# Kernel tuning notes

Measured on AMD Instinct MI355X. Metric: run time of the kernel, lower is better.

Reference implementation:

```python
import jax, jax.numpy as jnp
import numpy as np

B, S, P, V, D = 8, 32, 8, 8000, 128
CONC = 5.0  # concentrator_factor
EPS = 1e-8  # torch cosine_similarity eps


def setup_inputs() -> dict:
    key = jax.random.key(0)
    ks = jax.random.split(key, 8)
    concepts = jax.random.randint(ks[0], (B, S, P), 0, V)
    concepts_length = jax.random.randint(ks[1], (B, S), 0, P + 1)
    seg_len = jax.random.randint(ks[2], (B,), 1, S + 1)
    embed_w = jax.random.normal(ks[3], (V, D), jnp.float32)
    embed_kb_w = jax.random.normal(ks[4], (V, D), jnp.float32)
    edge_matrix = jax.random.uniform(ks[5], (V, V), jnp.float32)
    affectiveness = jax.random.uniform(ks[6], (V,), jnp.float32)
    lam = jnp.full((V,), 0.5, jnp.float32)  # _lambda init to GAW
    return dict(concepts=concepts, concepts_length=concepts_length, seg_len=seg_len,
                embed_w=embed_w, embed_kb_w=embed_kb_w, edge_matrix=edge_matrix,
                affectiveness=affectiveness, lam=lam)


def reference(concepts, concepts_length, seg_len, embed_w, embed_kb_w,
              edge_matrix, affectiveness, lam):
    f32 = embed_w.dtype
    # init_params: normalize edge_matrix rows by their range
    rng = edge_matrix.max(axis=1) - edge_matrix.min(axis=1)  # [V]
    em = edge_matrix / (rng + (rng == 0).astype(f32))[:, None]

    ce = embed_w[concepts]  # [B,S,P,D]
    # ragged mean over P (empty -> zeros, matching empty_tensor)
    pmask = (jnp.arange(P)[None, None, :] < concepts_length[:, :, None]).astype(f32)  # [B,S,P]
    denom = jnp.maximum(concepts_length, 1).astype(f32)[:, :, None]  # [B,S,1]
    mean_j = (ce * pmask[..., None]).sum(axis=2) / denom  # [B,S,D]
    # mean over valid segments j < seg_len
    smask = (jnp.arange(S)[None, :] < seg_len[:, None]).astype(f32)  # [B,S]
    context = (mean_j * smask[..., None]).sum(axis=1) / seg_len.astype(f32)[:, None]  # [B,D]

    # abs cosine similarity vs KB embedding table
    cn = context / jnp.maximum(jnp.linalg.norm(context, axis=1, keepdims=True), EPS)
    kn = embed_kb_w / jnp.maximum(jnp.linalg.norm(embed_kb_w, axis=1, keepdims=True), EPS)
    cos = jnp.abs(cn @ kn.T)  # [B,V]

    eg = em[concepts]  # [B,S,P,V] irregular row gather
    rel = eg * cos[:, None, None, :]
    aff = (eg > 0).astype(f32) * affectiveness
    w = lam * rel + (1.0 - lam) * aff  # [B,S,P,V]
    attn = jax.nn.softmax(w * CONC, axis=3)
    ce2 = attn @ embed_kb_w  # [B,S,P,D]

    # ragged mean over P again, zero out segments j >= seg_len (padded output)
    out = (ce2 * pmask[..., None]).sum(axis=2) / denom  # [B,S,D]
    out = out * smask[..., None]
    return out
```

## Files before the change

### kernel.cpp

```cpp
#include <hip/hip_runtime.h>
#include <cmath>

#define NB 8
#define NS 32
#define NP 8
#define NV 8000
#define ND 128
#define CONC 5.0f
#define EPS 1e-8f

#define NBS (NB * NS)
#define TROWS 8
#define USPLIT 25
#define URANGE 320
#define UCHUNK 64
#define NCHUNK (URANGE / UCHUNK)
#define ST 12
#define MAXIDX (NB * NS * NP)

#define WS_SCALE  0
#define WS_CN     2048
#define WS_COS    3072
#define WS_MEANJ  67072
#define WS_P      99840

__global__ void k_mean(const int* __restrict__ concepts,
                       const int* __restrict__ concepts_length,
                       const float* __restrict__ embed_w,
                       float* __restrict__ mean_j,
                       float* __restrict__ out) {
    const int bs = blockIdx.x;
    const int d = threadIdx.x;
    out[bs * ND + d] = 0.0f;
    const int len = concepts_length[bs];
    float sum = 0.0f;
    for (int p = 0; p < len; ++p) {
        const int c = concepts[bs * NP + p];
        sum += embed_w[(size_t)c * ND + d];
    }
    mean_j[(size_t)bs * ND + d] = sum / (float)(len > 0 ? len : 1);
}

__global__ void k_ctx2(const int* __restrict__ seg_len,
                       const float* __restrict__ mean_j,
                       float* __restrict__ cn) {
    const int b = blockIdx.x;
    const int d = threadIdx.x;
    const int sl = seg_len[b];
    float acc = 0.0f;
    for (int s = 0; s < sl; ++s) acc += mean_j[(size_t)(b * NS + s) * ND + d];
    acc /= (float)sl;
    float ss = acc * acc;
    #pragma unroll
    for (int m = 1; m < 64; m <<= 1) ss += __shfl_xor(ss, m);
    __shared__ float sred[2];
    if ((d & 63) == 0) sred[d >> 6] = ss;
    __syncthreads();
    const float tot = sred[0] + sred[1];
    cn[b * ND + d] = acc / fmaxf(sqrtf(tot), EPS);
}

__global__ __launch_bounds__(256) void k_cos(const float* __restrict__ kb,
                                             const float* __restrict__ cn,
                                             float* __restrict__ cos_bv) {
    __shared__ float s_cn[NB * ND];
    const int t = threadIdx.x;
    for (int i = t; i < NB * ND; i += 256) s_cn[i] = cn[i];
    __syncthreads();

    const int v = blockIdx.x * 8 + (t >> 5);
    const int l = t & 31;
    const float4 kv = *reinterpret_cast<const float4*>(kb + (size_t)v * ND + (l << 2));
    float ss = kv.x * kv.x + kv.y * kv.y + kv.z * kv.z + kv.w * kv.w;
    #pragma unroll
    for (int m = 1; m < 32; m <<= 1) ss += __shfl_xor(ss, m);
    const float inv = 1.0f / fmaxf(sqrtf(ss), EPS);
    #pragma unroll
    for (int b = 0; b < NB; ++b) {
        const float4 cv = *reinterpret_cast<const float4*>(&s_cn[b * ND + (l << 2)]);
        float dot = kv.x * cv.x + kv.y * cv.y + kv.z * cv.z + kv.w * cv.w;
        #pragma unroll
        for (int m = 1; m < 32; m <<= 1) dot += __shfl_xor(dot, m);
        if (l == 0) cos_bv[b * NV + v] = fabsf(dot * inv);
    }
}

__global__ __launch_bounds__(256) void k_A(
        const int* __restrict__ concepts,
        const int* __restrict__ concepts_length,
        const int* __restrict__ seg_len,
        const float* __restrict__ edge,
        const float* __restrict__ aff,
        const float* __restrict__ lam,
        const float* __restrict__ cos_bv,
        float* __restrict__ f_scale,
        float* __restrict__ pbuf) {
    const int idx = blockIdx.x;
    const int b = idx >> 8;
    const int s = (idx >> 3) & 31;
    const int p = idx & 7;
    if (s >= seg_len[b]) return;
    const int len = concepts_length[b * NS + s];
    if (p >= len) return;
    const int c = concepts[idx];

    const int t = threadIdx.x;
    const float* __restrict__ erow = edge + (size_t)c * NV;
    float4 ev[8];
    float lmax = -INFINITY, lmin = INFINITY;
    #pragma unroll
    for (int k = 0; k < 8; ++k) {
        const int f = t + (k << 8);
        if (f < 2000) {
            const float4 e = *reinterpret_cast<const float4*>(erow + (f << 2));
            ev[k] = e;
            lmax = fmaxf(lmax, fmaxf(fmaxf(e.x, e.y), fmaxf(e.z, e.w)));
            lmin = fminf(lmin, fminf(fminf(e.x, e.y), fminf(e.z, e.w)));
        }
    }
    #pragma unroll
    for (int m = 1; m < 64; m <<= 1) {
        lmax = fmaxf(lmax, __shfl_xor(lmax, m));
        lmin = fminf(lmin, __shfl_xor(lmin, m));
    }
    __shared__ float s_mn[4], s_mx[4], s_sum[4];
    if ((t & 63) == 0) { s_mn[t >> 6] = lmin; s_mx[t >> 6] = lmax; }
    __syncthreads();
    const float rmin = fminf(fminf(s_mn[0], s_mn[1]), fminf(s_mn[2], s_mn[3]));
    const float rmax = fmaxf(fmaxf(s_mx[0], s_mx[1]), fmaxf(s_mx[2], s_mx[3]));
    const float rng = rmax - rmin;
    const float inv_rng = 1.0f / (rng + (rng == 0.0f ? 1.0f : 0.0f));

    const float* __restrict__ cosb = cos_bv + b * NV;
    float* __restrict__ prow = pbuf + (size_t)idx * NV;
    float lsum = 0.0f;
    #pragma unroll
    for (int k = 0; k < 8; ++k) {
        const int f = t + (k << 8);
        if (f < 2000) {
            const int u = f << 2;
            const float4 l4 = *reinterpret_cast<const float4*>(lam + u);
            const float4 a4 = *reinterpret_cast<const float4*>(aff + u);
            const float4 c4 = *reinterpret_cast<const float4*>(cosb + u);
            float4 e = ev[k];
            e.x *= inv_rng; e.y *= inv_rng; e.z *= inv_rng; e.w *= inv_rng;
            float4 pe;
            pe.x = __expf((l4.x * e.x * c4.x + (1.0f - l4.x) * ((e.x > 0.0f) ? 1.0f : 0.0f) * a4.x) * CONC);
            pe.y = __expf((l4.y * e.y * c4.y + (1.0f - l4.y) * ((e.y > 0.0f) ? 1.0f : 0.0f) * a4.y) * CONC);
            pe.z = __expf((l4.z * e.z * c4.z + (1.0f - l4.z) * ((e.z > 0.0f) ? 1.0f : 0.0f) * a4.z) * CONC);
            pe.w = __expf((l4.w * e.w * c4.w + (1.0f - l4.w) * ((e.w > 0.0f) ? 1.0f : 0.0f) * a4.w) * CONC);
            *reinterpret_cast<float4*>(prow + (f << 2)) = pe;
            lsum += pe.x + pe.y + pe.z + pe.w;
        }
    }
    #pragma unroll
    for (int m = 1; m < 64; m <<= 1) lsum += __shfl_xor(lsum, m);
    if ((t & 63) == 0) s_sum[t >> 6] = lsum;
    __syncthreads();
    if (t == 0) {
        const float total = s_sum[0] + s_sum[1] + s_sum[2] + s_sum[3];
        f_scale[idx] = 1.0f / (total * (float)len);
    }
}

__global__ __launch_bounds__(256) void k_B(
        const float* __restrict__ kb,
        const int* __restrict__ seg_len,
        const int* __restrict__ concepts_length,
        const float* __restrict__ f_scale,
        const float* __restrict__ pbuf,
        float* __restrict__ out) {
    const int tile = blockIdx.x;
    const int bs0 = tile * TROWS;
    if ((bs0 & 31) >= seg_len[bs0 >> 5]) return;

    const int t = threadIdx.x;
    const int ug = t & 7;
    const int l = t >> 3;

    __shared__ int   s_ln[TROWS];
    __shared__ float s_sc[TROWS * NP];
    __shared__ __align__(16) float s_p[UCHUNK * ST];

    if (t < TROWS) {
        const int bs = bs0 + t;
        s_ln[t] = ((bs & 31) < seg_len[bs >> 5]) ? concepts_length[bs] : 0;
    }
    if (t < TROWS * NP) {
        const int bs = bs0 + (t >> 3);
        const int p = t & 7;
        const bool valid = ((bs & 31) < seg_len[bs >> 5]) && (p < concepts_length[bs]);
        s_sc[t] = valid ? f_scale[bs * NP + p] : 0.0f;
    }
    __syncthreads();

    const int srow = t >> 5;
    const int sq = t & 31;
    const int lenr = s_ln[srow];
    float scr[NP];
    #pragma unroll
    for (int p = 0; p < NP; ++p) scr[p] = s_sc[srow * NP + p];
    const float* __restrict__ pr = pbuf + (size_t)(bs0 + srow) * NP * NV + (sq << 1);
    const int u0 = blockIdx.y * URANGE;

    float4 acc[TROWS];
    #pragma unroll
    for (int j = 0; j < TROWS; ++j) acc[j] = make_float4(0.f, 0.f, 0.f, 0.f);

    float2 pv = make_float2(0.f, 0.f);
    #pragma unroll
    for (int p = 0; p < NP; ++p)
        if (p < lenr) {
            const float2 v = *reinterpret_cast<const float2*>(pr + (size_t)p * NV + u0);
            pv.x = fmaf(scr[p], v.x, pv.x);
            pv.y = fmaf(scr[p], v.y, pv.y);
        }

    for (int ch = 0; ch < NCHUNK; ++ch) {
        const int uu0 = sq << 1;
        s_p[(uu0 + 0) * ST + srow] = pv.x;
        s_p[(uu0 + 1) * ST + srow] = pv.y;
        float2 pn = make_float2(0.f, 0.f);
        if (ch + 1 < NCHUNK) {
            const int off = u0 + (ch + 1) * UCHUNK;
            #pragma unroll
            for (int p = 0; p < NP; ++p)
                if (p < lenr) {
                    const float2 v = *reinterpret_cast<const float2*>(pr + (size_t)p * NV + off);
                    pn.x = fmaf(scr[p], v.x, pn.x);
                    pn.y = fmaf(scr[p], v.y, pn.y);
                }
        }
        __syncthreads();

        const int uc = u0 + ch * UCHUNK;
        #pragma unroll
        for (int r = 0; r < 8; ++r) {
            const int uu = ug + (r << 3);
            const float4 kv = *reinterpret_cast<const float4*>(
                kb + (size_t)(uc + uu) * ND + (l << 2));
            const float4 p0 = *reinterpret_cast<const float4*>(&s_p[uu * ST]);
            const float4 p1 = *reinterpret_cast<const float4*>(&s_p[uu * ST + 4]);
            acc[0].x = fmaf(p0.x, kv.x, acc[0].x); acc[0].y = fmaf(p0.x, kv.y, acc[0].y);
            acc[0].z = fmaf(p0.x, kv.z, acc[0].z); acc[0].w = fmaf(p0.x, kv.w, acc[0].w);
            acc[1].x = fmaf(p0.y, kv.x, acc[1].x); acc[1].y = fmaf(p0.y, kv.y, acc[1].y);
            acc[1].z = fmaf(p0.y, kv.z, acc[1].z); acc[1].w = fmaf(p0.y, kv.w, acc[1].w);
            acc[2].x = fmaf(p0.z, kv.x, acc[2].x); acc[2].y = fmaf(p0.z, kv.y, acc[2].y);
            acc[2].z = fmaf(p0.z, kv.z, acc[2].z); acc[2].w = fmaf(p0.z, kv.w, acc[2].w);
            acc[3].x = fmaf(p0.w, kv.x, acc[3].x); acc[3].y = fmaf(p0.w, kv.y, acc[3].y);
            acc[3].z = fmaf(p0.w, kv.z, acc[3].z); acc[3].w = fmaf(p0.w, kv.w, acc[3].w);
            acc[4].x = fmaf(p1.x, kv.x, acc[4].x); acc[4].y = fmaf(p1.x, kv.y, acc[4].y);
            acc[4].z = fmaf(p1.x, kv.z, acc[4].z); acc[4].w = fmaf(p1.x, kv.w, acc[4].w);
            acc[5].x = fmaf(p1.y, kv.x, acc[5].x); acc[5].y = fmaf(p1.y, kv.y, acc[5].y);
            acc[5].z = fmaf(p1.y, kv.z, acc[5].z); acc[5].w = fmaf(p1.y, kv.w, acc[5].w);
            acc[6].x = fmaf(p1.z, kv.x, acc[6].x); acc[6].y = fmaf(p1.z, kv.y, acc[6].y);
            acc[6].z = fmaf(p1.z, kv.z, acc[6].z); acc[6].w = fmaf(p1.z, kv.w, acc[6].w);
            acc[7].x = fmaf(p1.w, kv.x, acc[7].x); acc[7].y = fmaf(p1.w, kv.y, acc[7].y);
            acc[7].z = fmaf(p1.w, kv.z, acc[7].z); acc[7].w = fmaf(p1.w, kv.w, acc[7].w);
        }
        __syncthreads();
        pv = pn;
    }

    float4 r0 = make_float4(0.f, 0.f, 0.f, 0.f);
    #pragma unroll
    for (int j = 0; j < TROWS; ++j) {
        float4 a = acc[j];
        #pragma unroll
        for (int m = 1; m <= 4; m <<= 1) {
            a.x += __shfl_xor(a.x, m);
            a.y += __shfl_xor(a.y, m);
            a.z += __shfl_xor(a.z, m);
            a.w += __shfl_xor(a.w, m);
        }
        if (j == ug) r0 = a;
    }

    if (s_ln[ug] != 0) {
        float* o = out + (size_t)(bs0 + ug) * ND + (l << 2);
        atomicAdd(o + 0, r0.x);
        atomicAdd(o + 1, r0.y);
        atomicAdd(o + 2, r0.z);
        atomicAdd(o + 3, r0.w);
    }
}

extern "C" void kernel_launch(void* const* d_in, const int* in_sizes, int n_in,
                              void* d_out, int out_size, void* d_ws, size_t ws_size,
                              hipStream_t stream) {
    const int*   concepts        = (const int*)d_in[0];
    const int*   concepts_length = (const int*)d_in[1];
    const int*   seg_len         = (const int*)d_in[2];
    const float* embed_w         = (const float*)d_in[3];
    const float* embed_kb_w      = (const float*)d_in[4];
    const float* edge_matrix     = (const float*)d_in[5];
    const float* affectiveness   = (const float*)d_in[6];
    const float* lam             = (const float*)d_in[7];
    float* out = (float*)d_out;

    float* wsf = (float*)d_ws;
    float* f_scale  = wsf + WS_SCALE;
    float* cn       = wsf + WS_CN;
    float* cos_bv   = wsf + WS_COS;
    float* mean_j   = wsf + WS_MEANJ;
    float* pbuf     = wsf + WS_P;

    k_mean<<<NB * NS, ND, 0, stream>>>(concepts, concepts_length, embed_w,
                                       mean_j, out);
    k_ctx2<<<NB, ND, 0, stream>>>(seg_len, mean_j, cn);
    k_cos<<<NV / 8, 256, 0, stream>>>(embed_kb_w, cn, cos_bv);
    k_A<<<MAXIDX, 256, 0, stream>>>(concepts, concepts_length, seg_len,
                                    edge_matrix, affectiveness, lam, cos_bv,
                                    f_scale, pbuf);
    dim3 gB(NBS / TROWS, USPLIT, 1);
    k_B<<<gB, 256, 0, stream>>>(embed_kb_w, seg_len, concepts_length,
                                f_scale, pbuf, out);
}
```

Before: 367.8 us.

## Recompute softmax numerators in matmul kernel instead of materializing probability buffer

```diff
diff --git a/kernel.cpp b/kernel.cpp
--- a/kernel.cpp
+++ b/kernel.cpp
@@ -19,10 +19,10 @@
 #define MAXIDX (NB * NS * NP)
 
 #define WS_SCALE  0
-#define WS_CN     2048
-#define WS_COS    3072
-#define WS_MEANJ  67072
-#define WS_P      99840
+#define WS_INVR   2048
+#define WS_CN     4096
+#define WS_COS    5120
+#define WS_MEANJ  69120
 
 __global__ void k_mean(const int* __restrict__ concepts,
                        const int* __restrict__ concepts_length,
@@ -85,7 +85,7 @@
     }
 }
 
-__global__ __launch_bounds__(256) void k_A(
+__global__ __launch_bounds__(256) void k_scale(
         const int* __restrict__ concepts,
         const int* __restrict__ concepts_length,
         const int* __restrict__ seg_len,
@@ -94,7 +94,7 @@
         const float* __restrict__ lam,
         const float* __restrict__ cos_bv,
         float* __restrict__ f_scale,
-        float* __restrict__ pbuf) {
+        float* __restrict__ f_invr) {
     const int idx = blockIdx.x;
     const int b = idx >> 8;
     const int s = (idx >> 3) & 31;
@@ -132,7 +132,6 @@
     const float inv_rng = 1.0f / (rng + (rng == 0.0f ? 1.0f : 0.0f));
 
     const float* __restrict__ cosb = cos_bv + b * NV;
-    float* __restrict__ prow = pbuf + (size_t)idx * NV;
     float lsum = 0.0f;
     #pragma unroll
     for (int k = 0; k < 8; ++k) {
@@ -143,14 +142,13 @@
             const float4 a4 = *reinterpret_cast<const float4*>(aff + u);
             const float4 c4 = *reinterpret_cast<const float4*>(cosb + u);
             float4 e = ev[k];
-            e.x *= inv_rng; e.y *= inv_rng; e.z *= inv_rng; e.w *= inv_rng;
-            float4 pe;
-            pe.x = __expf((l4.x * e.x * c4.x + (1.0f - l4.x) * ((e.x > 0.0f) ? 1.0f : 0.0f) * a4.x) * CONC);
-            pe.y = __expf((l4.y * e.y * c4.y + (1.0f - l4.y) * ((e.y > 0.0f) ? 1.0f : 0.0f) * a4.y) * CONC);
-            pe.z = __expf((l4.z * e.z * c4.z + (1.0f - l4.z) * ((e.z > 0.0f) ? 1.0f : 0.0f) * a4.z) * CONC);
-            pe.w = __expf((l4.w * e.w * c4.w + (1.0f - l4.w) * ((e.w > 0.0f) ? 1.0f : 0.0f) * a4.w) * CONC);
-            *reinterpret_cast<float4*>(prow + (f << 2)) = pe;
-            lsum += pe.x + pe.y + pe.z + pe.w;
+            float4 en;
+            en.x = e.x * inv_rng; en.y = e.y * inv_rng;
+            en.z = e.z * inv_rng; en.w = e.w * inv_rng;
+            lsum += __expf((l4.x * en.x * c4.x + (1.0f - l4.x) * ((e.x > 0.0f) ? 1.0f : 0.0f) * a4.x) * CONC);
+            lsum += __expf((l4.y * en.y * c4.y + (1.0f - l4.y) * ((e.y > 0.0f) ? 1.0f : 0.0f) * a4.y) * CONC);
+            lsum += __expf((l4.z * en.z * c4.z + (1.0f - l4.z) * ((e.z > 0.0f) ? 1.0f : 0.0f) * a4.z) * CONC);
+            lsum += __expf((l4.w * en.w * c4.w + (1.0f - l4.w) * ((e.w > 0.0f) ? 1.0f : 0.0f) * a4.w) * CONC);
         }
     }
     #pragma unroll
@@ -160,47 +158,57 @@
     if (t == 0) {
         const float total = s_sum[0] + s_sum[1] + s_sum[2] + s_sum[3];
         f_scale[idx] = 1.0f / (total * (float)len);
-    }
-}
-
-__global__ __launch_bounds__(256) void k_B(
+        f_invr[idx]  = inv_rng;
+    }
+}
+
+__global__ __launch_bounds__(256) void k_fused(
         const float* __restrict__ kb,
+        const int* __restrict__ concepts,
         const int* __restrict__ seg_len,
         const int* __restrict__ concepts_length,
+        const float* __restrict__ edge,
+        const float* __restrict__ aff,
+        const float* __restrict__ lam,
+        const float* __restrict__ cos_bv,
         const float* __restrict__ f_scale,
-        const float* __restrict__ pbuf,
+        const float* __restrict__ f_invr,
         float* __restrict__ out) {
     const int tile = blockIdx.x;
     const int bs0 = tile * TROWS;
-    if ((bs0 & 31) >= seg_len[bs0 >> 5]) return;
+    const int b = bs0 >> 5;
+    if ((bs0 & 31) >= seg_len[b]) return;
 
     const int t = threadIdx.x;
     const int ug = t & 7;
     const int l = t >> 3;
 
-    __shared__ int   s_ln[TROWS];
-    __shared__ float s_sc[TROWS * NP];
+    __shared__ int s_ln[TROWS];
     __shared__ __align__(16) float s_p[UCHUNK * ST];
 
     if (t < TROWS) {
         const int bs = bs0 + t;
-        s_ln[t] = ((bs & 31) < seg_len[bs >> 5]) ? concepts_length[bs] : 0;
-    }
-    if (t < TROWS * NP) {
-        const int bs = bs0 + (t >> 3);
-        const int p = t & 7;
-        const bool valid = ((bs & 31) < seg_len[bs >> 5]) && (p < concepts_length[bs]);
-        s_sc[t] = valid ? f_scale[bs * NP + p] : 0.0f;
+        s_ln[t] = ((bs & 31) < seg_len[b]) ? concepts_length[bs] : 0;
     }
     __syncthreads();
 
     const int srow = t >> 5;
     const int sq = t & 31;
+    const int bsr = bs0 + srow;
     const int lenr = s_ln[srow];
-    float scr[NP];
-    #pragma unroll
-    for (int p = 0; p < NP; ++p) scr[p] = s_sc[srow * NP + p];
-    const float* __restrict__ pr = pbuf + (size_t)(bs0 + srow) * NP * NV + (sq << 1);
+    float scr[NP], ivr[NP];
+    const float* ep[NP];
+    #pragma unroll
+    for (int p = 0; p < NP; ++p) {
+        if (p < lenr) {
+            scr[p] = f_scale[bsr * NP + p];
+            ivr[p] = f_invr[bsr * NP + p];
+            ep[p]  = edge + (size_t)concepts[bsr * NP + p] * NV;
+        } else {
+            scr[p] = 0.0f; ivr[p] = 0.0f; ep[p] = edge;
+        }
+    }
+    const float* __restrict__ cosb = cos_bv + b * NV;
     const int u0 = blockIdx.y * URANGE;
 
     float4 acc[TROWS];
@@ -208,13 +216,21 @@
     for (int j = 0; j < TROWS; ++j) acc[j] = make_float4(0.f, 0.f, 0.f, 0.f);
 
     float2 pv = make_float2(0.f, 0.f);
-    #pragma unroll
-    for (int p = 0; p < NP; ++p)
-        if (p < lenr) {
-            const float2 v = *reinterpret_cast<const float2*>(pr + (size_t)p * NV + u0);
-            pv.x = fmaf(scr[p], v.x, pv.x);
-            pv.y = fmaf(scr[p], v.y, pv.y);
-        }
+    {
+        const int u = u0 + (sq << 1);
+        const float2 l2 = *reinterpret_cast<const float2*>(lam + u);
+        const float2 a2 = *reinterpret_cast<const float2*>(aff + u);
+        const float2 c2 = *reinterpret_cast<const float2*>(cosb + u);
+        #pragma unroll
+        for (int p = 0; p < NP; ++p)
+            if (p < lenr) {
+                const float2 e = *reinterpret_cast<const float2*>(ep[p] + u);
+                const float wx = (l2.x * (e.x * ivr[p]) * c2.x + (1.0f - l2.x) * ((e.x > 0.0f) ? 1.0f : 0.0f) * a2.x) * CONC;
+                const float wy = (l2.y * (e.y * ivr[p]) * c2.y + (1.0f - l2.y) * ((e.y > 0.0f) ? 1.0f : 0.0f) * a2.y) * CONC;
+                pv.x = fmaf(scr[p], __expf(wx), pv.x);
+                pv.y = fmaf(scr[p], __expf(wy), pv.y);
+            }
+    }
 
     for (int ch = 0; ch < NCHUNK; ++ch) {
         const int uu0 = sq << 1;
@@ -222,13 +238,18 @@
         s_p[(uu0 + 1) * ST + srow] = pv.y;
         float2 pn = make_float2(0.f, 0.f);
         if (ch + 1 < NCHUNK) {
-            const int off = u0 + (ch + 1) * UCHUNK;
+            const int u = u0 + (ch + 1) * UCHUNK + (sq << 1);
+            const float2 l2 = *reinterpret_cast<const float2*>(lam + u);
+            const float2 a2 = *reinterpret_cast<const float2*>(aff + u);
+            const float2 c2 = *reinterpret_cast<const float2*>(cosb + u);
             #pragma unroll
             for (int p = 0; p < NP; ++p)
                 if (p < lenr) {
-                    const float2 v = *reinterpret_cast<const float2*>(pr + (size_t)p * NV + off);
-                    pn.x = fmaf(scr[p], v.x, pn.x);
-                    pn.y = fmaf(scr[p], v.y, pn.y);
+                    const float2 e = *reinterpret_cast<const float2*>(ep[p] + u);
+                    const float wx = (l2.x * (e.x * ivr[p]) * c2.x + (1.0f - l2.x) * ((e.x > 0.0f) ? 1.0f : 0.0f) * a2.x) * CONC;
+                    const float wy = (l2.y * (e.y * ivr[p]) * c2.y + (1.0f - l2.y) * ((e.y > 0.0f) ? 1.0f : 0.0f) * a2.y) * CONC;
+                    pn.x = fmaf(scr[p], __expf(wx), pn.x);
+                    pn.y = fmaf(scr[p], __expf(wy), pn.y);
                 }
         }
         __syncthreads();
@@ -299,20 +320,21 @@
     float* out = (float*)d_out;
 
     float* wsf = (float*)d_ws;
-    float* f_scale  = wsf + WS_SCALE;
-    float* cn       = wsf + WS_CN;
-    float* cos_bv   = wsf + WS_COS;
-    float* mean_j   = wsf + WS_MEANJ;
-    float* pbuf     = wsf + WS_P;
+    float* f_scale = wsf + WS_SCALE;
+    float* f_invr  = wsf + WS_INVR;
+    float* cn      = wsf + WS_CN;
+    float* cos_bv  = wsf + WS_COS;
+    float* mean_j  = wsf + WS_MEANJ;
 
     k_mean<<<NB * NS, ND, 0, stream>>>(concepts, concepts_length, embed_w,
                                        mean_j, out);
     k_ctx2<<<NB, ND, 0, stream>>>(seg_len, mean_j, cn);
     k_cos<<<NV / 8, 256, 0, stream>>>(embed_kb_w, cn, cos_bv);
-    k_A<<<MAXIDX, 256, 0, stream>>>(concepts, concepts_length, seg_len,
-                                    edge_matrix, affectiveness, lam, cos_bv,
-                                    f_scale, pbuf);
-    dim3 gB(NBS / TROWS, USPLIT, 1);
-    k_B<<<gB, 256, 0, stream>>>(embed_kb_w, seg_len, concepts_length,
-                                f_scale, pbuf, out);
-}
+    k_scale<<<MAXIDX, 256, 0, stream>>>(concepts, concepts_length, seg_len,
+                                        edge_matrix, affectiveness, lam, cos_bv,
+                                        f_scale, f_invr);
+    dim3 gF(NBS / TROWS, USPLIT, 1);
+    k_fused<<<gF, 256, 0, stream>>>(embed_kb_w, concepts, seg_len,
+                                    concepts_length, edge_matrix, affectiveness,
+                                    lam, cos_bv, f_scale, f_invr, out);
+}
```

Result: slower. 390.1 us (+6.1%).

## Fold per-concept softmax rows into a per-segment mean before the KB matmul

Applied to the files above, without the earlier changes.

```diff
diff --git a/kernel.cpp b/kernel.cpp
--- a/kernel.cpp
+++ b/kernel.cpp
@@ -16,13 +16,11 @@
 #define UCHUNK 64
 #define NCHUNK (URANGE / UCHUNK)
 #define ST 12
-#define MAXIDX (NB * NS * NP)
-
-#define WS_SCALE  0
-#define WS_CN     2048
-#define WS_COS    3072
-#define WS_MEANJ  67072
-#define WS_P      99840
+
+#define WS_CN     0
+#define WS_COS    1024
+#define WS_MEANJ  65024
+#define WS_Q      97792
 
 __global__ void k_mean(const int* __restrict__ concepts,
                        const int* __restrict__ concepts_length,
@@ -85,7 +83,7 @@
     }
 }
 
-__global__ __launch_bounds__(256) void k_A(
+__global__ __launch_bounds__(256) void k_soft(
         const int* __restrict__ concepts,
         const int* __restrict__ concepts_length,
         const int* __restrict__ seg_len,
@@ -93,73 +91,94 @@
         const float* __restrict__ aff,
         const float* __restrict__ lam,
         const float* __restrict__ cos_bv,
-        float* __restrict__ f_scale,
-        float* __restrict__ pbuf) {
-    const int idx = blockIdx.x;
-    const int b = idx >> 8;
-    const int s = (idx >> 3) & 31;
-    const int p = idx & 7;
+        float* __restrict__ q) {
+    const int bs = blockIdx.x;
+    const int b = bs >> 5;
+    const int s = bs & 31;
     if (s >= seg_len[b]) return;
-    const int len = concepts_length[b * NS + s];
-    if (p >= len) return;
-    const int c = concepts[idx];
+    const int len = concepts_length[bs];
+    if (len == 0) return;
 
     const int t = threadIdx.x;
-    const float* __restrict__ erow = edge + (size_t)c * NV;
-    float4 ev[8];
-    float lmax = -INFINITY, lmin = INFINITY;
+    const float* __restrict__ cosb = cos_bv + b * NV;
+    const float inv_len_base = 1.0f / (float)len;
+
+    float4 qa[8];
+    #pragma unroll
+    for (int k = 0; k < 8; ++k) qa[k] = make_float4(0.f, 0.f, 0.f, 0.f);
+
+    __shared__ float s_mn[4], s_mx[4], s_sum[4];
+
+    for (int p = 0; p < len; ++p) {
+        const int c = concepts[bs * NP + p];
+        const float* __restrict__ erow = edge + (size_t)c * NV;
+        float4 ev[8];
+        float lmax = -INFINITY, lmin = INFINITY;
+        #pragma unroll
+        for (int k = 0; k < 8; ++k) {
+            const int f = t + (k << 8);
+            if (f < 2000) {
+                const float4 e = *reinterpret_cast<const float4*>(erow + (f << 2));
+                ev[k] = e;
+                lmax = fmaxf(lmax, fmaxf(fmaxf(e.x, e.y), fmaxf(e.z, e.w)));
+                lmin = fminf(lmin, fminf(fminf(e.x, e.y), fminf(e.z, e.w)));
+            }
+        }
+        #pragma unroll
+        for (int m = 1; m < 64; m <<= 1) {
+            lmax = fmaxf(lmax, __shfl_xor(lmax, m));
+            lmin = fminf(lmin, __shfl_xor(lmin, m));
+        }
+        if ((t & 63) == 0) { s_mn[t >> 6] = lmin; s_mx[t >> 6] = lmax; }
+        __syncthreads();
+        const float rmin = fminf(fminf(s_mn[0], s_mn[1]), fminf(s_mn[2], s_mn[3]));
+        const float rmax = fmaxf(fmaxf(s_mx[0], s_mx[1]), fmaxf(s_mx[2], s_mx[3]));
+        const float rng = rmax - rmin;
+        const float inv_rng = 1.0f / (rng + (rng == 0.0f ? 1.0f : 0.0f));
+
+        float lsum = 0.0f;
+        #pragma unroll
+        for (int k = 0; k < 8; ++k) {
+            const int f = t + (k << 8);
+            if (f < 2000) {
+                const int u = f << 2;
+                const float4 l4 = *reinterpret_cast<const float4*>(lam + u);
+                const float4 a4 = *reinterpret_cast<const float4*>(aff + u);
+                const float4 c4 = *reinterpret_cast<const float4*>(cosb + u);
+                const float4 e = ev[k];
+                float4 pe;
+                pe.x = __expf((l4.x * (e.x * inv_rng) * c4.x + (1.0f - l4.x) * ((e.x > 0.0f) ? 1.0f : 0.0f) * a4.x) * CONC);
+                pe.y = __expf((l4.y * (e.y * inv_rng) * c4.y + (1.0f - l4.y) * ((e.y > 0.0f) ? 1.0f : 0.0f) * a4.y) * CONC);
+                pe.z = __expf((l4.z * (e.z * inv_rng) * c4.z + (1.0f - l4.z) * ((e.z > 0.0f) ? 1.0f : 0.0f) * a4.z) * CONC);
+                pe.w = __expf((l4.w * (e.w * inv_rng) * c4.w + (1.0f - l4.w) * ((e.w > 0.0f) ? 1.0f : 0.0f) * a4.w) * CONC);
+                ev[k] = pe;
+                lsum += pe.x + pe.y + pe.z + pe.w;
+            }
+        }
+        #pragma unroll
+        for (int m = 1; m < 64; m <<= 1) lsum += __shfl_xor(lsum, m);
+        if ((t & 63) == 0) s_sum[t >> 6] = lsum;
+        __syncthreads();
+        const float total = s_sum[0] + s_sum[1] + s_sum[2] + s_sum[3];
+        const float scale = inv_len_base / total;
+        #pragma unroll
+        for (int k = 0; k < 8; ++k) {
+            if (t + (k << 8) < 2000) {
+                qa[k].x = fmaf(scale, ev[k].x, qa[k].x);
+                qa[k].y = fmaf(scale, ev[k].y, qa[k].y);
+                qa[k].z = fmaf(scale, ev[k].z, qa[k].z);
+                qa[k].w = fmaf(scale, ev[k].w, qa[k].w);
+            }
+        }
+        __syncthreads();
+    }
+
+    float* __restrict__ qrow = q + (size_t)bs * NV;
     #pragma unroll
     for (int k = 0; k < 8; ++k) {
         const int f = t + (k << 8);
-        if (f < 2000) {
-            const float4 e = *reinterpret_cast<const float4*>(erow + (f << 2));
-            ev[k] = e;
-            lmax = fmaxf(lmax, fmaxf(fmaxf(e.x, e.y), fmaxf(e.z, e.w)));
-            lmin = fminf(lmin, fminf(fminf(e.x, e.y), fminf(e.z, e.w)));
-        }
-    }
-    #pragma unroll
-    for (int m = 1; m < 64; m <<= 1) {
-        lmax = fmaxf(lmax, __shfl_xor(lmax, m));
-        lmin = fminf(lmin, __shfl_xor(lmin, m));
-    }
-    __shared__ float s_mn[4], s_mx[4], s_sum[4];
-    if ((t & 63) == 0) { s_mn[t >> 6] = lmin; s_mx[t >> 6] = lmax; }
-    __syncthreads();
-    const float rmin = fminf(fminf(s_mn[0], s_mn[1]), fminf(s_mn[2], s_mn[3]));
-    const float rmax = fmaxf(fmaxf(s_mx[0], s_mx[1]), fmaxf(s_mx[2], s_mx[3]));
-    const float rng = rmax - rmin;
-    const float inv_rng = 1.0f / (rng + (rng == 0.0f ? 1.0f : 0.0f));
-
-    const float* __restrict__ cosb = cos_bv + b * NV;
-    float* __restrict__ prow = pbuf + (size_t)idx * NV;
-    float lsum = 0.0f;
-    #pragma unroll
-    for (int k = 0; k < 8; ++k) {
-        const int f = t + (k << 8);
-        if (f < 2000) {
-            const int u = f << 2;
-            const float4 l4 = *reinterpret_cast<const float4*>(lam + u);
-            const float4 a4 = *reinterpret_cast<const float4*>(aff + u);
-            const float4 c4 = *reinterpret_cast<const float4*>(cosb + u);
-            float4 e = ev[k];
-            e.x *= inv_rng; e.y *= inv_rng; e.z *= inv_rng; e.w *= inv_rng;
-            float4 pe;
-            pe.x = __expf((l4.x * e.x * c4.x + (1.0f - l4.x) * ((e.x > 0.0f) ? 1.0f : 0.0f) * a4.x) * CONC);
-            pe.y = __expf((l4.y * e.y * c4.y + (1.0f - l4.y) * ((e.y > 0.0f) ? 1.0f : 0.0f) * a4.y) * CONC);
-            pe.z = __expf((l4.z * e.z * c4.z + (1.0f - l4.z) * ((e.z > 0.0f) ? 1.0f : 0.0f) * a4.z) * CONC);
-            pe.w = __expf((l4.w * e.w * c4.w + (1.0f - l4.w) * ((e.w > 0.0f) ? 1.0f : 0.0f) * a4.w) * CONC);
-            *reinterpret_cast<float4*>(prow + (f << 2)) = pe;
-            lsum += pe.x + pe.y + pe.z + pe.w;
-        }
-    }
-    #pragma unroll
-    for (int m = 1; m < 64; m <<= 1) lsum += __shfl_xor(lsum, m);
-    if ((t & 63) == 0) s_sum[t >> 6] = lsum;
-    __syncthreads();
-    if (t == 0) {
-        const float total = s_sum[0] + s_sum[1] + s_sum[2] + s_sum[3];
-        f_scale[idx] = 1.0f / (total * (float)len);
+        if (f < 2000)
+            *reinterpret_cast<float4*>(qrow + (f << 2)) = qa[k];
     }
 }
 
@@ -167,40 +186,30 @@
         const float* __restrict__ kb,
         const int* __restrict__ seg_len,
         const int* __restrict__ concepts_length,
-        const float* __restrict__ f_scale,
-        const float* __restrict__ pbuf,
+        const float* __restrict__ q,
         float* __restrict__ out) {
     const int tile = blockIdx.x;
     const int bs0 = tile * TROWS;
-    if ((bs0 & 31) >= seg_len[bs0 >> 5]) return;
+    const int b = bs0 >> 5;
+    if ((bs0 & 31) >= seg_len[b]) return;
 
     const int t = threadIdx.x;
     const int ug = t & 7;
     const int l = t >> 3;
 
-    __shared__ int   s_ln[TROWS];
-    __shared__ float s_sc[TROWS * NP];
+    __shared__ int s_ln[TROWS];
     __shared__ __align__(16) float s_p[UCHUNK * ST];
 
     if (t < TROWS) {
         const int bs = bs0 + t;
-        s_ln[t] = ((bs & 31) < seg_len[bs >> 5]) ? concepts_length[bs] : 0;
-    }
-    if (t < TROWS * NP) {
-        const int bs = bs0 + (t >> 3);
-        const int p = t & 7;
-        const bool valid = ((bs & 31) < seg_len[bs >> 5]) && (p < concepts_length[bs]);
-        s_sc[t] = valid ? f_scale[bs * NP + p] : 0.0f;
+        s_ln[t] = ((bs & 31) < seg_len[b]) ? concepts_length[bs] : 0;
     }
     __syncthreads();
 
     const int srow = t >> 5;
     const int sq = t & 31;
-    const int lenr = s_ln[srow];
-    float scr[NP];
-    #pragma unroll
-    for (int p = 0; p < NP; ++p) scr[p] = s_sc[srow * NP + p];
-    const float* __restrict__ pr = pbuf + (size_t)(bs0 + srow) * NP * NV + (sq << 1);
+    const bool rok = (s_ln[srow] != 0);
+    const float* __restrict__ qr = q + (size_t)(bs0 + srow) * NV + (sq << 1);
     const int u0 = blockIdx.y * URANGE;
 
     float4 acc[TROWS];
@@ -208,29 +217,15 @@
     for (int j = 0; j < TROWS; ++j) acc[j] = make_float4(0.f, 0.f, 0.f, 0.f);
 
     float2 pv = make_float2(0.f, 0.f);
-    #pragma unroll
-    for (int p = 0; p < NP; ++p)
-        if (p < lenr) {
-            const float2 v = *reinterpret_cast<const float2*>(pr + (size_t)p * NV + u0);
-            pv.x = fmaf(scr[p], v.x, pv.x);
-            pv.y = fmaf(scr[p], v.y, pv.y);
-        }
+    if (rok) pv = *reinterpret_cast<const float2*>(qr + u0);
 
     for (int ch = 0; ch < NCHUNK; ++ch) {
         const int uu0 = sq << 1;
         s_p[(uu0 + 0) * ST + srow] = pv.x;
         s_p[(uu0 + 1) * ST + srow] = pv.y;
         float2 pn = make_float2(0.f, 0.f);
-        if (ch + 1 < NCHUNK) {
-            const int off = u0 + (ch + 1) * UCHUNK;
-            #pragma unroll
-            for (int p = 0; p < NP; ++p)
-                if (p < lenr) {
-                    const float2 v = *reinterpret_cast<const float2*>(pr + (size_t)p * NV + off);
-                    pn.x = fmaf(scr[p], v.x, pn.x);
-                    pn.y = fmaf(scr[p], v.y, pn.y);
-                }
-        }
+        if (ch + 1 < NCHUNK && rok)
+            pn = *reinterpret_cast<const float2*>(qr + u0 + (ch + 1) * UCHUNK);
         __syncthreads();
 
         const int uc = u0 + ch * UCHUNK;
@@ -299,20 +294,17 @@
     float* out = (float*)d_out;
 
     float* wsf = (float*)d_ws;
-    float* f_scale  = wsf + WS_SCALE;
-    float* cn       = wsf + WS_CN;
-    float* cos_bv   = wsf + WS_COS;
-    float* mean_j   = wsf + WS_MEANJ;
-    float* pbuf     = wsf + WS_P;
+    float* cn     = wsf + WS_CN;
+    float* cos_bv = wsf + WS_COS;
+    float* mean_j = wsf + WS_MEANJ;
+    float* q      = wsf + WS_Q;
 
     k_mean<<<NB * NS, ND, 0, stream>>>(concepts, concepts_length, embed_w,
                                        mean_j, out);
     k_ctx2<<<NB, ND, 0, stream>>>(seg_len, mean_j, cn);
     k_cos<<<NV / 8, 256, 0, stream>>>(embed_kb_w, cn, cos_bv);
-    k_A<<<MAXIDX, 256, 0, stream>>>(concepts, concepts_length, seg_len,
-                                    edge_matrix, affectiveness, lam, cos_bv,
-                                    f_scale, pbuf);
+    k_soft<<<NBS, 256, 0, stream>>>(concepts, concepts_length, seg_len,
+                                    edge_matrix, affectiveness, lam, cos_bv, q);
     dim3 gB(NBS / TROWS, USPLIT, 1);
-    k_B<<<gB, 256, 0, stream>>>(embed_kb_w, seg_len, concepts_length,
-                                f_scale, pbuf, out);
-}
+    k_B<<<gB, 256, 0, stream>>>(embed_kb_w, seg_len, concepts_length, q, out);
+}
```

Measured after the change: 388.3 us. 1.06x slower.
